# Optimization experiments

Hardware: AMD Instinct MI355X
Metric: run time of the kernel (lower is better)

The kernel has to match this reference:

```python
import jax, jax.numpy as jnp
import numpy as np

L = 7
D = 20
V = 2 ** L                      # voxel_size
NUM_EMB = V ** 3
DOM_LO, DOM_HI = -1.0, 1.0
DOM_LEN = DOM_HI - DOM_LO

# 8 corner offsets in the order used by the torch module
OFFSETS = jnp.array([[0, 0, 0], [1, 0, 0], [0, 1, 0], [1, 1, 0],
                     [0, 0, 1], [1, 0, 1], [0, 1, 1], [1, 1, 1]], dtype=jnp.int32)


def setup_inputs() -> dict:
    key = jax.random.key(0)
    kx, kg = jax.random.split(key)
    # points strictly inside the domain so floor()+1 corner stays in-range
    x = jax.random.uniform(kx, (1_000_000, 3), jnp.float32, minval=-1.0, maxval=0.998)
    grid = jax.random.normal(kg, (NUM_EMB, D), jnp.float32) * 0.02  # embedding table
    return {"x": x, "grid": grid}


def reference(x, grid):
    # points -> grid space, floor to lower corner
    gp = jnp.floor((x - DOM_LO) / DOM_LEN * V)                  # [P,3] float
    grid_idx = gp[:, None, :].astype(jnp.int32) + OFFSETS[None]  # [P,8,3]
    # flat index: ix * V^0 + iy * V^1 + iz * V^2
    flat = grid_idx[..., 0] + grid_idx[..., 1] * V + grid_idx[..., 2] * (V * V)
    Q_emb = grid[flat]                                          # [P,8,D] gather
    Q_pos = grid_idx.astype(x.dtype) / V * DOM_LEN + DOM_LO      # [P,8,3] world pos

    px, py, pz = x[:, 0], x[:, 1], x[:, 2]
    x1, x2 = Q_pos[:, 0, 0], Q_pos[:, 1, 0]
    y1, y2 = Q_pos[:, 0, 1], Q_pos[:, 2, 1]
    z1, z2 = Q_pos[:, 0, 2], Q_pos[:, 4, 2]

    q000, q100, q010, q110 = Q_emb[:, 0], Q_emb[:, 1], Q_emb[:, 2], Q_emb[:, 3]
    q001, q101, q011, q111 = Q_emb[:, 4], Q_emb[:, 5], Q_emb[:, 6], Q_emb[:, 7]

    wx0 = ((x2 - px) / (x2 - x1))[:, None]
    wx1 = ((px - x1) / (x2 - x1))[:, None]
    fx0 = wx0 * q000 + wx1 * q100
    fx1 = wx0 * q010 + wx1 * q110
    fx2 = wx0 * q001 + wx1 * q101
    fx3 = wx0 * q011 + wx1 * q111

    wy0 = ((y2 - py) / (y2 - y1))[:, None]
    wy1 = ((py - y1) / (y2 - y1))[:, None]
    fy0 = wy0 * fx0 + wy1 * fx1
    fy1 = wy0 * fx2 + wy1 * fx3

    wz0 = ((z2 - pz) / (z2 - z1))[:, None]
    wz1 = ((pz - z1) / (z2 - z1))[:, None]
    return wz0 * fy0 + wz1 * fy1                                 # [P,D]
```

## Files before the change

kernel.cpp:

```cpp
#include <hip/hip_runtime.h>

#define V 128
#define D 20
#define NUM_EMB (V * V * V)

typedef float v4f __attribute__((ext_vector_type(4)));

__global__ __launch_bounds__(320) void dense_grid_enc_kernel(
    const float* __restrict__ x, const float* __restrict__ grid,
    float* __restrict__ out, int N)
{
    int tid = threadIdx.x;
    int lp  = tid / 5;
    int k   = tid - lp * 5;
    int i   = blockIdx.x * 64 + lp;
    if (i >= N) return;

    float px = x[3 * i + 0];
    float py = x[3 * i + 1];
    float pz = x[3 * i + 2];

    int ix = (int)floorf((px + 1.0f) * 64.0f);
    int iy = (int)floorf((py + 1.0f) * 64.0f);
    int iz = (int)floorf((pz + 1.0f) * 64.0f);

    int f000 = ix + iy * V + iz * V * V;

    int flats[8];
    flats[0] = f000;
    flats[1] = f000 + 1;
    flats[2] = f000 + V;
    flats[3] = f000 + V + 1;
    flats[4] = f000 + V * V;
    flats[5] = f000 + V * V + 1;
    flats[6] = f000 + V * V + V;
    flats[7] = f000 + V * V + V + 1;
    #pragma unroll
    for (int c = 0; c < 8; c++) {
        if (flats[c] > NUM_EMB - 1) flats[c] = NUM_EMB - 1;
    }

    const char* gbase = (const char*)grid;
    unsigned koff = (unsigned)(16 * k);

    v4f q[8];
    #pragma unroll
    for (int c = 0; c < 8; c++) {
        unsigned off = (unsigned)flats[c] * 80u + koff;
        q[c] = *(const v4f*)(gbase + (size_t)off);
    }

    float x1 = (float)ix * (2.0f / 128.0f) - 1.0f;
    float y1 = (float)iy * (2.0f / 128.0f) - 1.0f;
    float z1 = (float)iz * (2.0f / 128.0f) - 1.0f;
    float x2 = x1 + (2.0f / 128.0f);
    float y2 = y1 + (2.0f / 128.0f);
    float z2 = z1 + (2.0f / 128.0f);

    float wx[2], wy[2], wz[2];
    wx[1] = (px - x1) * 64.0f; wx[0] = (x2 - px) * 64.0f;
    wy[1] = (py - y1) * 64.0f; wy[0] = (y2 - py) * 64.0f;
    wz[1] = (pz - z1) * 64.0f; wz[0] = (z2 - pz) * 64.0f;

    __builtin_amdgcn_sched_barrier(0);

    v4f acc = (v4f)(0.0f);
    #pragma unroll
    for (int c = 0; c < 8; c++) {
        float w = wx[c & 1] * wy[(c >> 1) & 1] * wz[(c >> 2) & 1];
        acc += w * q[c];
    }

    __builtin_nontemporal_store(acc, (v4f*)(out + (size_t)i * D + 4 * k));
}

extern "C" void kernel_launch(void* const* d_in, const int* in_sizes, int n_in,
                              void* d_out, int out_size, void* d_ws, size_t ws_size,
                              hipStream_t stream) {
    const float* x = (const float*)d_in[0];
    const float* grid = (const float*)d_in[1];
    float* out = (float*)d_out;
    int N = in_sizes[0] / 3;

    int pts_per_block = 64;
    int nblocks = (N + pts_per_block - 1) / pts_per_block;
    dense_grid_enc_kernel<<<nblocks, 320, 0, stream>>>(x, grid, out, N);
}
```

Baseline: 360.5 us.

## Gather grid corners into LDS via global_load_lds in a persistent wave loop

Restructures the kernel so each wave handles groups of 8 points, with one lane per (point, corner) pair. Each lane issues 16-byte global_load_lds transfers straight into LDS, and 40 lanes then read those slabs back to interpolate and store the output. The launch changes to a fixed grid-stride loop of 2048 blocks of 256 threads. The intent is fewer gather instructions and fewer address registers per point. The cost is an extra LDS round trip, only 40 of 64 lanes active during compute, and a serial wait on each group with no pipelining between groups.

```diff
diff --git a/kernel.cpp b/kernel.cpp
--- a/kernel.cpp
+++ b/kernel.cpp
@@ -6,72 +6,84 @@
 
 typedef float v4f __attribute__((ext_vector_type(4)));
 
-__global__ __launch_bounds__(320) void dense_grid_enc_kernel(
+typedef const __attribute__((address_space(1))) void gv_t;
+typedef __attribute__((address_space(3))) void lv_t;
+#define G2L(gsrc, ldst) \
+    __builtin_amdgcn_global_load_lds((gv_t*)(gsrc), (lv_t*)(ldst), 16, 0, 0)
+
+__global__ __launch_bounds__(256) void dense_grid_enc_kernel(
     const float* __restrict__ x, const float* __restrict__ grid,
     float* __restrict__ out, int N)
 {
-    int tid = threadIdx.x;
-    int lp  = tid / 5;
-    int k   = tid - lp * 5;
-    int i   = blockIdx.x * 64 + lp;
-    if (i >= N) return;
+    __shared__ float lds[4 * 5 * 256];
 
-    float px = x[3 * i + 0];
-    float py = x[3 * i + 1];
-    float pz = x[3 * i + 2];
+    const int tid  = threadIdx.x;
+    const int wave = tid >> 6;
+    const int lane = tid & 63;
+    float* wlds = &lds[wave * 5 * 256];
 
-    int ix = (int)floorf((px + 1.0f) * 64.0f);
-    int iy = (int)floorf((py + 1.0f) * 64.0f);
-    int iz = (int)floorf((pz + 1.0f) * 64.0f);
+    const int sp = lane >> 3;
+    const int sc = lane & 7;
+    const int cp = lane / 5;
+    const int ck = lane - cp * 5;
+    const int csrc = (cp & 7) * 8;
 
-    int f000 = ix + iy * V + iz * V * V;
+    const int ngroups = (N + 7) >> 3;
+    const int nwaves  = (int)gridDim.x * 4;
 
-    int flats[8];
-    flats[0] = f000;
-    flats[1] = f000 + 1;
-    flats[2] = f000 + V;
-    flats[3] = f000 + V + 1;
-    flats[4] = f000 + V * V;
-    flats[5] = f000 + V * V + 1;
-    flats[6] = f000 + V * V + V;
-    flats[7] = f000 + V * V + V + 1;
-    #pragma unroll
-    for (int c = 0; c < 8; c++) {
-        if (flats[c] > NUM_EMB - 1) flats[c] = NUM_EMB - 1;
+    for (int g = blockIdx.x * 4 + wave; g < ngroups; g += nwaves) {
+        const int gbase = g << 3;
+
+        int i_s = gbase + sp;
+        if (i_s > N - 1) i_s = N - 1;
+        float px = x[3 * i_s + 0];
+        float py = x[3 * i_s + 1];
+        float pz = x[3 * i_s + 2];
+        int ix = (int)floorf((px + 1.0f) * 64.0f);
+        int iy = (int)floorf((py + 1.0f) * 64.0f);
+        int iz = (int)floorf((pz + 1.0f) * 64.0f);
+        int f = ix + iy * V + iz * (V * V)
+              + (sc & 1) + ((sc >> 1) & 1) * V + ((sc >> 2) & 1) * (V * V);
+        if (f > NUM_EMB - 1) f = NUM_EMB - 1;
+        const float* gp = grid + (size_t)f * D;
+
+        G2L(gp,      wlds + 0 * 256);
+        G2L(gp + 4,  wlds + 1 * 256);
+        G2L(gp + 8,  wlds + 2 * 256);
+        G2L(gp + 12, wlds + 3 * 256);
+        G2L(gp + 16, wlds + 4 * 256);
+
+        float qx = __shfl(px, csrc, 64);
+        float qy = __shfl(py, csrc, 64);
+        float qz = __shfl(pz, csrc, 64);
+
+        __builtin_amdgcn_s_waitcnt(0x0F70);
+        __builtin_amdgcn_sched_barrier(0);
+
+        if (lane < 40) {
+            float gx = (qx + 1.0f) * 64.0f;
+            float gy = (qy + 1.0f) * 64.0f;
+            float gz = (qz + 1.0f) * 64.0f;
+            float fx = gx - floorf(gx);
+            float fy = gy - floorf(gy);
+            float fz = gz - floorf(gz);
+
+            const float* slab = wlds + ck * 256;
+            v4f acc = (v4f)(0.0f);
+            #pragma unroll
+            for (int j = 0; j < 8; j++) {
+                int c = (j + cp + ck) & 7;
+                v4f q = *(const v4f*)(slab + (cp * 8 + c) * 4);
+                float w = ((c & 1) ? fx : 1.0f - fx)
+                        * (((c >> 1) & 1) ? fy : 1.0f - fy)
+                        * (((c >> 2) & 1) ? fz : 1.0f - fz);
+                acc += w * q;
+            }
+            int i = gbase + cp;
+            if (i < N)
+                __builtin_nontemporal_store(acc, (v4f*)(out + (size_t)i * D + ck * 4));
+        }
     }
-
-    const char* gbase = (const char*)grid;
-    unsigned koff = (unsigned)(16 * k);
-
-    v4f q[8];
-    #pragma unroll
-    for (int c = 0; c < 8; c++) {
-        unsigned off = (unsigned)flats[c] * 80u + koff;
-        q[c] = *(const v4f*)(gbase + (size_t)off);
-    }
-
-    float x1 = (float)ix * (2.0f / 128.0f) - 1.0f;
-    float y1 = (float)iy * (2.0f / 128.0f) - 1.0f;
-    float z1 = (float)iz * (2.0f / 128.0f) - 1.0f;
-    float x2 = x1 + (2.0f / 128.0f);
-    float y2 = y1 + (2.0f / 128.0f);
-    float z2 = z1 + (2.0f / 128.0f);
-
-    float wx[2], wy[2], wz[2];
-    wx[1] = (px - x1) * 64.0f; wx[0] = (x2 - px) * 64.0f;
-    wy[1] = (py - y1) * 64.0f; wy[0] = (y2 - py) * 64.0f;
-    wz[1] = (pz - z1) * 64.0f; wz[0] = (z2 - pz) * 64.0f;
-
-    __builtin_amdgcn_sched_barrier(0);
-
-    v4f acc = (v4f)(0.0f);
-    #pragma unroll
-    for (int c = 0; c < 8; c++) {
-        float w = wx[c & 1] * wy[(c >> 1) & 1] * wz[(c >> 2) & 1];
-        acc += w * q[c];
-    }
-
-    __builtin_nontemporal_store(acc, (v4f*)(out + (size_t)i * D + 4 * k));
 }
 
 extern "C" void kernel_launch(void* const* d_in, const int* in_sizes, int n_in,
@@ -82,7 +94,8 @@
     float* out = (float*)d_out;
     int N = in_sizes[0] / 3;
 
-    int pts_per_block = 64;
-    int nblocks = (N + pts_per_block - 1) / pts_per_block;
-    dense_grid_enc_kernel<<<nblocks, 320, 0, stream>>>(x, grid, out, N);
+    int ngroups = (N + 7) / 8;
+    int nblocks = 2048;
+    if (nblocks > ngroups) nblocks = ngroups;
+    dense_grid_enc_kernel<<<nblocks, 256, 0, stream>>>(x, grid, out, N);
 }
```

Measured after the change: 396.2 us. 1.1x slower.
